# Kernel tuning notes

Hardware: AMD Instinct MI355X
Metric: run time of the kernel (lower is better)

## Reference

```python
import jax, jax.numpy as jnp
import numpy as np

S = 4096          # sequence length (must equal d_model due to the module's v-transpose bug)
D = 4096          # d_model; n_head = heads = 1, bs = 1
SCALE = 64.0      # scale_factor = sqrt(d_model)
W_STD = 0.02      # weight init scale to keep softmax logits sane


def setup_inputs() -> dict:
    k0 = jax.random.key(0)
    ks = jax.random.split(k0, 8)
    return {
        "query": jax.random.normal(ks[0], (1, S, D), jnp.float32),
        "key":   jax.random.normal(ks[1], (1, S, D), jnp.float32),
        "value": jax.random.normal(ks[2], (1, S, D), jnp.float32),
        "Wq": jax.random.normal(ks[3], (D, D), jnp.float32) * W_STD,
        "bq": jnp.zeros((D,), jnp.float32),
        "Wk": jax.random.normal(ks[4], (D, D), jnp.float32) * W_STD,
        "bk": jnp.zeros((D,), jnp.float32),
        "Wv": jax.random.normal(ks[5], (D, D), jnp.float32) * W_STD,
        "bv": jnp.zeros((D,), jnp.float32),
        "Wo": jax.random.normal(ks[6], (D, D), jnp.float32) * W_STD,
        "bo": jnp.zeros((D,), jnp.float32),
    }


def reference(query, key, value, Wq, bq, Wk, bk, Wv, bv, Wo, bo):
    # Linear projections (torch Linear: x @ W.T + b). n_head = 1, so out dim = D.
    q = query @ Wq.T + bq                       # [1, S, D]
    k = key   @ Wk.T + bk                       # [1, S, D]
    v = value @ Wv.T + bv                       # [1, S, D]
    # k.reshape(bs, heads, -1, d_model).transpose(2, 3) -> [1, 1, D, S]
    k4 = k.reshape(1, 1, S, D).transpose(0, 1, 3, 2)
    # v gets the SAME (buggy) transpose -> [1, 1, D, S]
    v4 = v.reshape(1, 1, S, D).transpose(0, 1, 3, 2)
    # q [1,S,D] broadcasts against k4 [1,1,D,S] -> scores [1,1,S,S]
    scores = jnp.matmul(q[:, None], k4) / SCALE
    attn = jax.nn.softmax(scores, axis=-1)      # [1, 1, S, S]
    # dropout_p = 0 / eval mode -> identity
    ctx = jnp.matmul(attn, v4)                  # [1, 1, S, D] (S == D)
    out = ctx @ Wo.T + bo + value[:, None]      # residual add, broadcast to [1,1,S,D]
    return out.reshape(1, -1, D)                # [1, S, D]
```

## Files before the change

### kernel.cpp

```cpp
#include <hip/hip_runtime.h>


typedef __attribute__((ext_vector_type(4))) float f32x4;
typedef __attribute__((ext_vector_type(8))) short short8;
typedef __attribute__((ext_vector_type(4))) unsigned short us4;

#define DIM 4096
#define NT  64

__device__ __forceinline__ unsigned short f2bf(float f) {
    unsigned int u = __builtin_bit_cast(unsigned int, f);
    u += 0x7fffu + ((u >> 16) & 1u);
    return (unsigned short)(u >> 16);
}

__device__ __forceinline__ float bf2f(unsigned short h) {
    return __builtin_bit_cast(float, (unsigned int)h << 16);
}

__device__ __forceinline__ void gll16(const void* g, void* l) {
    __builtin_amdgcn_global_load_lds(
        (const __attribute__((address_space(1))) unsigned int*)g,
        (__attribute__((address_space(3))) unsigned int*)l,
        16, 0, 0);
}

__global__ void cast_kernel(const float* __restrict__ in, unsigned short* __restrict__ out) {
    const size_t i = ((size_t)blockIdx.x * 256 + threadIdx.x) * 4;
    float4 x = *(const float4*)(in + i);
    us4 y;
    y.x = f2bf(x.x); y.y = f2bf(x.y); y.z = f2bf(x.z); y.w = f2bf(x.w);
    *(us4*)(out + i) = y;
}

template <int EPI>
__global__ __launch_bounds__(512, 2)
void gemm256(const unsigned short* __restrict__ A, const unsigned short* __restrict__ B,
             void* __restrict__ Cout, const float* __restrict__ bias,
             const unsigned short* __restrict__ resb, const float* __restrict__ rowscale) {
    __shared__ alignas(16) char lds[131072];

    const int tid = threadIdx.x;
    const int w = tid >> 6, l = tid & 63;
    const int wr = w >> 2, wc = w & 3;

    const int bid = blockIdx.x;
    const int swz = (bid & 7) * 32 + (bid >> 3);
    const int row0 = (swz >> 4) << 8;
    const int col0 = (swz & 15) << 8;

    const int laneA  = (l & 15) * 64 + (((l >> 4) << 4) ^ ((l & 8) << 2));
    const int sl_row = l >> 2;
    const int sl_col = ((l & 3) << 3) ^ ((l & 32) ? 16 : 0);

    f32x4 acc[8][4];
    const f32x4 zero = {0.f, 0.f, 0.f, 0.f};
#pragma unroll
    for (int m = 0; m < 8; ++m)
#pragma unroll
        for (int n = 0; n < 4; ++n) acc[m][n] = zero;

    char* const ldsp = (char*)lds;
    char* const A0 = ldsp;
    char* const B0 = ldsp + 32768;
    char* const A1 = ldsp + 65536;
    char* const B1 = ldsp + 98304;

    const int aoff = wr * 16384 + laneA;
    const int boff = wc * 8192 + laneA;

    auto stage = [&](const unsigned short* __restrict__ M, char* ldsMat, int rowbase,
                     int t, int h) {
        {
            const int rg = h * 8 + (w >> 1), cg = w & 1;
            gll16(M + (size_t)(rowbase + rg * 16 + sl_row) * DIM + t * 64 + cg * 32 + sl_col,
                  ldsMat + ((rg * 2 + cg) << 10));
        }
        {
            const int s = 8 + w;
            const int rg = h * 8 + (s >> 1), cg = s & 1;
            gll16(M + (size_t)(rowbase + rg * 16 + sl_row) * DIM + t * 64 + cg * 32 + sl_col,
                  ldsMat + ((rg * 2 + cg) << 10));
        }
    };

    short8 alo[4][2], ahi[4][2], b0[2][2], b1[2][2];

    stage(A, A0, row0, 0, 0); stage(A, A0, row0, 0, 1);
    stage(B, B0, col0, 0, 0); stage(B, B0, col0, 0, 1);
    stage(A, A1, row0, 1, 0); stage(A, A1, row0, 1, 1);
    stage(B, B1, col0, 1, 0); stage(B, B1, col0, 1, 1);
    asm volatile("s_waitcnt vmcnt(8)\ns_barrier" ::: "memory");
#pragma unroll
    for (int m2 = 0; m2 < 4; ++m2)
#pragma unroll
        for (int ks = 0; ks < 2; ++ks)
            alo[m2][ks] = *(const short8*)(A0 + aoff + ((m2 * 2 + ks) << 10));
#pragma unroll
    for (int n2 = 0; n2 < 2; ++n2)
#pragma unroll
        for (int ks = 0; ks < 2; ++ks)
            b0[n2][ks] = *(const short8*)(B0 + boff + ((n2 * 2 + ks) << 10));

    auto body = [&](int t, char* Abuf, char* Bbuf, const char* An, const char* Bn) {
        const int t2 = (t + 2 < NT) ? t + 2 : NT - 1;

#pragma unroll
        for (int m2 = 0; m2 < 4; ++m2)
#pragma unroll
            for (int ks = 0; ks < 2; ++ks)
                ahi[m2][ks] = *(const short8*)(Abuf + aoff + (((4 + m2) * 2 + ks) << 10));
        __builtin_amdgcn_s_setprio(1);
#pragma unroll
        for (int m2 = 0; m2 < 4; ++m2)
#pragma unroll
            for (int n2 = 0; n2 < 2; ++n2)
#pragma unroll
                for (int ks = 0; ks < 2; ++ks)
                    acc[m2][n2] = __builtin_amdgcn_mfma_f32_16x16x32_bf16(
                        alo[m2][ks], b0[n2][ks], acc[m2][n2], 0, 0, 0);
        __builtin_amdgcn_s_setprio(0);

#pragma unroll
        for (int n2 = 0; n2 < 2; ++n2)
#pragma unroll
            for (int ks = 0; ks < 2; ++ks)
                b1[n2][ks] = *(const short8*)(Bbuf + boff + (((2 + n2) * 2 + ks) << 10));
        __builtin_amdgcn_s_setprio(1);
#pragma unroll
        for (int m2 = 0; m2 < 4; ++m2)
#pragma unroll
            for (int n2 = 0; n2 < 2; ++n2)
#pragma unroll
                for (int ks = 0; ks < 2; ++ks)
                    acc[4 + m2][n2] = __builtin_amdgcn_mfma_f32_16x16x32_bf16(
                        ahi[m2][ks], b0[n2][ks], acc[4 + m2][n2], 0, 0, 0);
        __builtin_amdgcn_s_setprio(0);
        asm volatile("s_waitcnt vmcnt(0)\ns_barrier" ::: "memory");

#pragma unroll
        for (int n2 = 0; n2 < 2; ++n2)
#pragma unroll
            for (int ks = 0; ks < 2; ++ks)
                b0[n2][ks] = *(const short8*)(Bn + boff + ((n2 * 2 + ks) << 10));
        stage(A, Abuf, row0, t2, 0);
        stage(B, Bbuf, col0, t2, 0);
        __builtin_amdgcn_s_setprio(1);
#pragma unroll
        for (int m2 = 0; m2 < 4; ++m2)
#pragma unroll
            for (int n2 = 0; n2 < 2; ++n2)
#pragma unroll
                for (int ks = 0; ks < 2; ++ks)
                    acc[m2][2 + n2] = __builtin_amdgcn_mfma_f32_16x16x32_bf16(
                        alo[m2][ks], b1[n2][ks], acc[m2][2 + n2], 0, 0, 0);
        __builtin_amdgcn_s_setprio(0);

#pragma unroll
        for (int m2 = 0; m2 < 4; ++m2)
#pragma unroll
            for (int ks = 0; ks < 2; ++ks)
                alo[m2][ks] = *(const short8*)(An + aoff + ((m2 * 2 + ks) << 10));
        stage(A, Abuf, row0, t2, 1);
        stage(B, Bbuf, col0, t2, 1);
        __builtin_amdgcn_s_setprio(1);
#pragma unroll
        for (int m2 = 0; m2 < 4; ++m2)
#pragma unroll
            for (int n2 = 0; n2 < 2; ++n2)
#pragma unroll
                for (int ks = 0; ks < 2; ++ks)
                    acc[4 + m2][2 + n2] = __builtin_amdgcn_mfma_f32_16x16x32_bf16(
                        ahi[m2][ks], b1[n2][ks], acc[4 + m2][2 + n2], 0, 0, 0);
        __builtin_amdgcn_s_setprio(0);
    };

#pragma unroll 1
    for (int tt = 0; tt < NT / 2; ++tt) {
        const int t = 2 * tt;
        body(t,     A0, B0, A1, B1);
        body(t + 1, A1, B1, A0, B0);
    }
    asm volatile("s_waitcnt vmcnt(0)" ::: "memory");

#pragma unroll
    for (int mf = 0; mf < 8; ++mf) {
        const int grow0 = row0 + wr * 128 + mf * 16 + ((l >> 4) << 2);
#pragma unroll
        for (int nf = 0; nf < 4; ++nf) {
            const int gcol = col0 + wc * 64 + nf * 16 + (l & 15);
            float bias_v = 0.f;
            if constexpr (EPI == 0 || EPI == 2) {
                bias_v = bias[gcol];
            }
#pragma unroll
            for (int r = 0; r < 4; ++r) {
                const int grow = grow0 + r;
                const size_t idx = (size_t)grow * DIM + gcol;
                const float a = acc[mf][nf][r];
                if constexpr (EPI == 0) {
                    ((unsigned short*)Cout)[idx] = f2bf(a + bias_v);
                } else if constexpr (EPI == 1) {
                    ((unsigned short*)Cout)[idx] = f2bf(__expf(a * 0.015625f));
                } else if constexpr (EPI == 2) {
                    ((float*)Cout)[idx] = a + bias_v + bf2f(resb[idx]);
                } else {
                    ((unsigned short*)Cout)[idx] = f2bf(a * rowscale[grow]);
                }
            }
        }
    }
}

__global__ __launch_bounds__(256)
void rowsum_kernel(const unsigned short* __restrict__ E, float* __restrict__ invs) {
    const int row = blockIdx.x;
    const int t = threadIdx.x;
    const unsigned short* src = E + (size_t)row * DIM + t * 16;

    float s = 0.f;
#pragma unroll
    for (int j = 0; j < 2; ++j) {
        short8 v = *(const short8*)(src + j * 8);
#pragma unroll
        for (int e = 0; e < 8; ++e)
            s += bf2f((unsigned short)v[e]);
    }
#pragma unroll
    for (int off = 32; off > 0; off >>= 1) s += __shfl_xor(s, off);

    __shared__ float red[4];
    if ((t & 63) == 0) red[t >> 6] = s;
    __syncthreads();
    if (t == 0) {
        const float tot = (red[0] + red[1]) + (red[2] + red[3]);
        invs[row] = 1.0f / tot;
    }
}

extern "C" void kernel_launch(void* const* d_in, const int* in_sizes, int n_in,
                              void* d_out, int out_size, void* d_ws, size_t ws_size,
                              hipStream_t stream) {
    const float* query = (const float*)d_in[0];
    const float* key   = (const float*)d_in[1];
    const float* value = (const float*)d_in[2];
    const float* Wq    = (const float*)d_in[3];
    const float* bq    = (const float*)d_in[4];
    const float* Wk    = (const float*)d_in[5];
    const float* bk    = (const float*)d_in[6];
    const float* Wv    = (const float*)d_in[7];
    const float* bv    = (const float*)d_in[8];
    const float* Wo    = (const float*)d_in[9];
    const float* bo    = (const float*)d_in[10];

    const size_t SZ = (size_t)DIM * DIM;
    unsigned short* qb   = (unsigned short*)d_ws;
    unsigned short* kb   = qb + SZ;
    unsigned short* vb   = kb + SZ;
    unsigned short* xb   = vb + SZ;
    unsigned short* wb   = xb + SZ;
    unsigned short* Eb   = wb + SZ;
    unsigned short* ctxb = Eb + SZ;
    float* invs = (float*)(ctxb + SZ);

    const dim3 cg(16384), cb(256);
    const dim3 gg(256), gb(512);

    cast_kernel<<<cg, cb, 0, stream>>>(query, xb);
    cast_kernel<<<cg, cb, 0, stream>>>(Wq, wb);
    gemm256<0><<<gg, gb, 0, stream>>>(xb, wb, qb, bq, nullptr, nullptr);
    cast_kernel<<<cg, cb, 0, stream>>>(key, xb);
    cast_kernel<<<cg, cb, 0, stream>>>(Wk, wb);
    gemm256<0><<<gg, gb, 0, stream>>>(xb, wb, kb, bk, nullptr, nullptr);
    cast_kernel<<<cg, cb, 0, stream>>>(value, xb);
    cast_kernel<<<cg, cb, 0, stream>>>(Wv, wb);
    gemm256<0><<<gg, gb, 0, stream>>>(xb, wb, vb, bv, nullptr, nullptr);
    gemm256<1><<<gg, gb, 0, stream>>>(qb, kb, Eb, nullptr, nullptr, nullptr);
    rowsum_kernel<<<4096, 256, 0, stream>>>(Eb, invs);
    gemm256<3><<<gg, gb, 0, stream>>>(Eb, vb, ctxb, nullptr, nullptr, invs);
    cast_kernel<<<cg, cb, 0, stream>>>(Wo, wb);
    gemm256<2><<<gg, gb, 0, stream>>>(ctxb, wb, d_out, bo, xb, nullptr);
}
```

Measured before the change: 793.3 us.

## Fuse softmax row-sum into QK^T GEMM epilogue and drop block swizzle

Computes per-row partial sums of the exponentiated scores inside the QK^T GEMM epilogue, using shuffles and LDS, and writes 16 partials per row. A small kernel then reduces them into inverse sums. This replaces a separate pass that re-read the whole bf16 score matrix. It also removes the block-index swizzle from all GEMMs, which may change L2 reuse, and adds 4 KB of LDS.

```diff
diff --git a/kernel.cpp b/kernel.cpp
--- a/kernel.cpp
+++ b/kernel.cpp
@@ -37,17 +37,17 @@
 __global__ __launch_bounds__(512, 2)
 void gemm256(const unsigned short* __restrict__ A, const unsigned short* __restrict__ B,
              void* __restrict__ Cout, const float* __restrict__ bias,
-             const unsigned short* __restrict__ resb, const float* __restrict__ rowscale) {
-    __shared__ alignas(16) char lds[131072];
+             const unsigned short* __restrict__ resb, const float* __restrict__ rowscale,
+             float* __restrict__ partial) {
+    __shared__ alignas(16) char lds[131072 + 4096];
 
     const int tid = threadIdx.x;
     const int w = tid >> 6, l = tid & 63;
     const int wr = w >> 2, wc = w & 3;
 
     const int bid = blockIdx.x;
-    const int swz = (bid & 7) * 32 + (bid >> 3);
-    const int row0 = (swz >> 4) << 8;
-    const int col0 = (swz & 15) << 8;
+    const int row0 = (bid >> 4) << 8;
+    const int col0 = (bid & 15) << 8;
 
     const int laneA  = (l & 15) * 64 + (((l >> 4) << 4) ^ ((l & 8) << 2));
     const int sl_row = l >> 2;
@@ -65,6 +65,7 @@
     char* const B0 = ldsp + 32768;
     char* const A1 = ldsp + 65536;
     char* const B1 = ldsp + 98304;
+    float* const smem = (float*)(ldsp + 131072);
 
     const int aoff = wr * 16384 + laneA;
     const int boff = wc * 8192 + laneA;
@@ -183,9 +184,11 @@
     }
     asm volatile("s_waitcnt vmcnt(0)" ::: "memory");
 
+    if constexpr (EPI == 1) __syncthreads();
 #pragma unroll
     for (int mf = 0; mf < 8; ++mf) {
         const int grow0 = row0 + wr * 128 + mf * 16 + ((l >> 4) << 2);
+        float rs[4] = {0.f, 0.f, 0.f, 0.f};
 #pragma unroll
         for (int nf = 0; nf < 4; ++nf) {
             const int gcol = col0 + wc * 64 + nf * 16 + (l & 15);
@@ -201,7 +204,9 @@
                 if constexpr (EPI == 0) {
                     ((unsigned short*)Cout)[idx] = f2bf(a + bias_v);
                 } else if constexpr (EPI == 1) {
-                    ((unsigned short*)Cout)[idx] = f2bf(__expf(a * 0.015625f));
+                    const float e = __expf(a * 0.015625f);
+                    rs[r] += e;
+                    ((unsigned short*)Cout)[idx] = f2bf(e);
                 } else if constexpr (EPI == 2) {
                     ((float*)Cout)[idx] = a + bias_v + bf2f(resb[idx]);
                 } else {
@@ -209,33 +214,34 @@
                 }
             }
         }
+        if constexpr (EPI == 1) {
+#pragma unroll
+            for (int r = 0; r < 4; ++r) {
+                float s = rs[r];
+                s += __shfl_xor(s, 1); s += __shfl_xor(s, 2);
+                s += __shfl_xor(s, 4); s += __shfl_xor(s, 8);
+                if ((l & 15) == 0)
+                    smem[wc * 256 + wr * 128 + mf * 16 + ((l >> 4) << 2) + r] = s;
+            }
+        }
     }
+    if constexpr (EPI == 1) {
+        __syncthreads();
+        if (tid < 256) {
+            const float s = smem[tid] + smem[256 + tid] + smem[512 + tid] + smem[768 + tid];
+            partial[(size_t)(col0 >> 8) * DIM + row0 + tid] = s;
+        }
+    }
 }
 
 __global__ __launch_bounds__(256)
-void rowsum_kernel(const unsigned short* __restrict__ E, float* __restrict__ invs) {
-    const int row = blockIdx.x;
-    const int t = threadIdx.x;
-    const unsigned short* src = E + (size_t)row * DIM + t * 16;
-
+void invs_kernel(const float* __restrict__ partial, float* __restrict__ invs) {
+    const int row = blockIdx.x * 256 + threadIdx.x;
     float s = 0.f;
 #pragma unroll
-    for (int j = 0; j < 2; ++j) {
-        short8 v = *(const short8*)(src + j * 8);
-#pragma unroll
-        for (int e = 0; e < 8; ++e)
-            s += bf2f((unsigned short)v[e]);
-    }
-#pragma unroll
-    for (int off = 32; off > 0; off >>= 1) s += __shfl_xor(s, off);
-
-    __shared__ float red[4];
-    if ((t & 63) == 0) red[t >> 6] = s;
-    __syncthreads();
-    if (t == 0) {
-        const float tot = (red[0] + red[1]) + (red[2] + red[3]);
-        invs[row] = 1.0f / tot;
-    }
+    for (int cb = 0; cb < 16; ++cb)
+        s += partial[(size_t)cb * DIM + row];
+    invs[row] = 1.0f / s;
 }
 
 extern "C" void kernel_launch(void* const* d_in, const int* in_sizes, int n_in,
@@ -261,23 +267,24 @@
     unsigned short* wb   = xb + SZ;
     unsigned short* Eb   = wb + SZ;
     unsigned short* ctxb = Eb + SZ;
-    float* invs = (float*)(ctxb + SZ);
+    float* invs    = (float*)(ctxb + SZ);
+    float* partial = invs + DIM;
 
     const dim3 cg(16384), cb(256);
     const dim3 gg(256), gb(512);
 
     cast_kernel<<<cg, cb, 0, stream>>>(query, xb);
     cast_kernel<<<cg, cb, 0, stream>>>(Wq, wb);
-    gemm256<0><<<gg, gb, 0, stream>>>(xb, wb, qb, bq, nullptr, nullptr);
+    gemm256<0><<<gg, gb, 0, stream>>>(xb, wb, qb, bq, nullptr, nullptr, nullptr);
     cast_kernel<<<cg, cb, 0, stream>>>(key, xb);
     cast_kernel<<<cg, cb, 0, stream>>>(Wk, wb);
-    gemm256<0><<<gg, gb, 0, stream>>>(xb, wb, kb, bk, nullptr, nullptr);
+    gemm256<0><<<gg, gb, 0, stream>>>(xb, wb, kb, bk, nullptr, nullptr, nullptr);
     cast_kernel<<<cg, cb, 0, stream>>>(value, xb);
     cast_kernel<<<cg, cb, 0, stream>>>(Wv, wb);
-    gemm256<0><<<gg, gb, 0, stream>>>(xb, wb, vb, bv, nullptr, nullptr);
-    gemm256<1><<<gg, gb, 0, stream>>>(qb, kb, Eb, nullptr, nullptr, nullptr);
-    rowsum_kernel<<<4096, 256, 0, stream>>>(Eb, invs);
-    gemm256<3><<<gg, gb, 0, stream>>>(Eb, vb, ctxb, nullptr, nullptr, invs);
+    gemm256<0><<<gg, gb, 0, stream>>>(xb, wb, vb, bv, nullptr, nullptr, nullptr);
+    gemm256<1><<<gg, gb, 0, stream>>>(qb, kb, Eb, nullptr, nullptr, nullptr, partial);
+    invs_kernel<<<16, 256, 0, stream>>>(partial, invs);
+    gemm256<3><<<gg, gb, 0, stream>>>(Eb, vb, ctxb, nullptr, nullptr, invs, nullptr);
     cast_kernel<<<cg, cb, 0, stream>>>(Wo, wb);
-    gemm256<2><<<gg, gb, 0, stream>>>(ctxb, wb, d_out, bo, xb, nullptr);
-}
+    gemm256<2><<<gg, gb, 0, stream>>>(ctxb, wb, d_out, bo, xb, nullptr, nullptr);
+}
```

Measured after the change: 790.6 us. Within noise of the previous version (-0.3%).
